# Optimization experiments

Hardware: AMD Instinct MI355X
Metric: run time of the kernel (lower is better)

## Reference

```python
import jax, jax.numpy as jnp
import numpy as np

NR_EMB = 1024
B_COMMITMENT = 1.0


def setup_inputs() -> dict:
    key = jax.random.key(0)
    k1, k2 = jax.random.split(key)
    inpt = jax.random.normal(k1, (64, 2048, 64), dtype=jnp.float32)
    # VarianceScaling(uniform) over shape (D, K): limit = sqrt(3*scale/fan_in), scale=1, fan_in=D
    D = 64
    limit = np.sqrt(3.0 / D).astype(np.float32)
    emb_mtrx = jax.random.uniform(k2, (D, NR_EMB), dtype=jnp.float32, minval=-limit, maxval=limit)
    return {"inpt": inpt, "emb_mtrx": emb_mtrx}


def reference(inpt, emb_mtrx):
    D = inpt.shape[-1]
    x = inpt.reshape(-1, D)  # [N, D]
    dist = (jnp.sum(x * x, axis=1, keepdims=True)
            - 2.0 * (x @ emb_mtrx)
            + jnp.sum(emb_mtrx * emb_mtrx, axis=0, keepdims=True))
    idx = jnp.argmax(-dist, axis=1)  # [N]
    # avg_probs = mean of one-hot over N == normalized histogram (same math, no N x K one-hot)
    avg_probs = jnp.bincount(idx, length=NR_EMB).astype(inpt.dtype) / x.shape[0]
    perplexity = jnp.exp(-jnp.sum(avg_probs * jnp.log(avg_probs + 1e-10)))
    idx_nd = idx.reshape(inpt.shape[:-1])  # [B, T]
    q = jnp.take(emb_mtrx.T, idx_nd, axis=0)  # gather codebook rows -> [B, T, D]
    l_commitment = jnp.mean((jax.lax.stop_gradient(q) - inpt) ** 2)
    l_codebook = jnp.mean((q - jax.lax.stop_gradient(inpt)) ** 2)
    loss = B_COMMITMENT * l_commitment + l_codebook
    q = inpt + jax.lax.stop_gradient(q - inpt)  # straight-through estimator
    return q, loss, perplexity
```

## Files before the change

### kernel.cpp

```cpp
#include <hip/hip_runtime.h>

#define NROWS 131072
#define D 64
#define K 1024

typedef __attribute__((ext_vector_type(8))) short short8;
typedef __attribute__((ext_vector_type(4))) float f32x4;
typedef unsigned int u32;


__device__ __forceinline__ unsigned short f2bf_rne(float f) {
    u32 u = __float_as_uint(f);
    u += 0x7fff + ((u >> 16) & 1);
    return (unsigned short)(u >> 16);
}

__device__ __forceinline__ float b2f(short s) {
    return __uint_as_float(((u32)(unsigned short)s) << 16);
}

__global__ __launch_bounds__(256) void prep_kernel(const float* __restrict__ E,
                                                   unsigned short* __restrict__ ehT,
                                                   float* __restrict__ e2g,
                                                   int* __restrict__ hist) {
    __shared__ float ps[4][64];
    const int lane = threadIdx.x & 63;
    const int w = threadIdx.x >> 6;
    const int k = blockIdx.x * 64 + lane;
    float s = 0.f;
#pragma unroll
    for (int half = 0; half < 2; ++half) {
        short8 h8;
#pragma unroll
        for (int j = 0; j < 8; ++j) {
            float v = E[(w * 16 + half * 8 + j) * K + k];
            s = fmaf(v, v, s);
            h8[j] = (short)f2bf_rne(v);
        }
        *(short8*)(ehT + (size_t)k * D + w * 16 + half * 8) = h8;
    }
    ps[w][lane] = s;
    __syncthreads();
    if (w == 0) e2g[k] = -0.5f * (ps[0][lane] + ps[1][lane] + ps[2][lane] + ps[3][lane]);
    if (threadIdx.x < 64) hist[blockIdx.x * 64 + threadIdx.x] = 0;
}

__global__ __launch_bounds__(256) void score_kernel(const float* __restrict__ X,
                                                    const unsigned short* __restrict__ ehT,
                                                    const float* __restrict__ e2g,
                                                    int* __restrict__ hist,
                                                    float* __restrict__ wavesum,
                                                    float* __restrict__ q) {
    __shared__ unsigned short xbuf[8192];
    __shared__ float mrg[128 * 5];
    __shared__ int idxl[128];
    __shared__ float redL[4];

    const int tid = threadIdx.x;
    const int wave = tid >> 6;
    const int lane = tid & 63;
    const int quad = lane >> 4;
    const int lc = lane & 15;
    const size_t row0 = (size_t)blockIdx.x * 128;

#pragma unroll
    for (int j = 0; j < 4; ++j) {
        int u = tid + j * 256;
        int tt = u >> 7, oo = (u >> 4) & 7, ll = u & 15;
        const float* xp = X + (row0 + (size_t)(tt * 16 + ll)) * D + oo * 8;
        float4 La = *(const float4*)(xp);
        float4 Lb = *(const float4*)(xp + 4);
        union { u32 uu[4]; short8 v; } pk;
        pk.uu[0] = __builtin_amdgcn_perm(__float_as_uint(La.y), __float_as_uint(La.x), 0x07060302);
        pk.uu[1] = __builtin_amdgcn_perm(__float_as_uint(La.w), __float_as_uint(La.z), 0x07060302);
        pk.uu[2] = __builtin_amdgcn_perm(__float_as_uint(Lb.y), __float_as_uint(Lb.x), 0x07060302);
        pk.uu[3] = __builtin_amdgcn_perm(__float_as_uint(Lb.w), __float_as_uint(Lb.z), 0x07060302);
        *(short8*)((char*)&xbuf[0] + u * 16) = pk.v;
    }
    __syncthreads();

    float bt8[8];
#pragma unroll
    for (int t = 0; t < 8; ++t) bt8[t] = -3.4e38f;

#pragma unroll 1
    for (int h = 0; h < 4; ++h) {
        const int cg = h * 256 + wave * 64;
        short8 ae[4][2];
        f32x4 e2f[4];
#pragma unroll
        for (int ct = 0; ct < 4; ++ct) {
            const unsigned short* ap = ehT + ((size_t)(cg + ct * 16 + lc) << 6) + quad * 8;
            ae[ct][0] = *(const short8*)(ap);
            ae[ct][1] = *(const short8*)(ap + 32);
            e2f[ct] = *(const f32x4*)(e2g + cg + ct * 16 + quad * 4);
        }
        const u32 cb0 = (u32)(cg + quad * 4);

#pragma unroll 2
        for (int t = 0; t < 8; ++t) {
            const char* bp = (const char*)&xbuf[0] + t * 2048 + quad * 256 + lc * 16;
            short8 b0 = *(const short8*)(bp);
            short8 b1 = *(const short8*)(bp + 1024);
            float bt = bt8[t];
#pragma unroll
            for (int ct = 0; ct < 4; ++ct) {
                f32x4 acc = __builtin_amdgcn_mfma_f32_16x16x32_bf16(ae[ct][0], b0, e2f[ct], 0, 0, 0);
                acc = __builtin_amdgcn_mfma_f32_16x16x32_bf16(ae[ct][1], b1, acc, 0, 0, 0);
                float p0 = __uint_as_float((__float_as_uint(acc[0]) & 0xFFFFFC00u) | (cb0 + ct * 16 + 0));
                float p1 = __uint_as_float((__float_as_uint(acc[1]) & 0xFFFFFC00u) | (cb0 + ct * 16 + 1));
                float p2 = __uint_as_float((__float_as_uint(acc[2]) & 0xFFFFFC00u) | (cb0 + ct * 16 + 2));
                float p3 = __uint_as_float((__float_as_uint(acc[3]) & 0xFFFFFC00u) | (cb0 + ct * 16 + 3));
                bt = fmaxf(bt, fmaxf(p0, p1));
                bt = fmaxf(bt, fmaxf(p2, p3));
            }
            bt8[t] = bt;
        }
    }

#pragma unroll
    for (int t = 0; t < 8; ++t) {
        float bt = bt8[t];
        bt = fmaxf(bt, __shfl_xor(bt, 16, 64));
        bt = fmaxf(bt, __shfl_xor(bt, 32, 64));
        if (lane < 16) mrg[(t * 16 + lane) * 5 + wave] = bt;
    }
    __syncthreads();

    if (tid < 128) {
        float m = fmaxf(fmaxf(mrg[tid * 5 + 0], mrg[tid * 5 + 1]),
                        fmaxf(mrg[tid * 5 + 2], mrg[tid * 5 + 3]));
        int kk = (int)(__float_as_uint(m) & 1023u);
        idxl[tid] = kk;
        atomicAdd(&hist[kk], 1);
    }
    __syncthreads();

    float ls = 0.f;
    const int er = tid >> 4, el = tid & 15;
#pragma unroll 2
    for (int it = 0; it < 8; ++it) {
        int rl = it * 16 + er;
        int k = idxl[rl];
        size_t row = row0 + rl;
        float4 xv = *(const float4*)(X + row * D + el * 4);
        short4 ev = *(const short4*)((const char*)ehT + (size_t)k * 128 + el * 8);
        float4 o;
        float dd;
        dd = b2f(ev.x) - xv.x; ls = fmaf(dd, dd, ls); o.x = xv.x + dd;
        dd = b2f(ev.y) - xv.y; ls = fmaf(dd, dd, ls); o.y = xv.y + dd;
        dd = b2f(ev.z) - xv.z; ls = fmaf(dd, dd, ls); o.z = xv.z + dd;
        dd = b2f(ev.w) - xv.w; ls = fmaf(dd, dd, ls); o.w = xv.w + dd;
        *(float4*)(q + row * D + el * 4) = o;
    }
    for (int off = 32; off > 0; off >>= 1) ls += __shfl_down(ls, off, 64);
    if (lane == 0) redL[wave] = ls;
    __syncthreads();
    if (tid == 0)
        wavesum[blockIdx.x] = redL[0] + redL[1] + redL[2] + redL[3];
}

__global__ __launch_bounds__(1024) void finalize_kernel(const int* __restrict__ hist,
                                                        const float* __restrict__ wavesum,
                                                        float* __restrict__ out) {
    __shared__ float redH[16], redL[16];
    int tid = threadIdx.x;
    float p = (float)hist[tid] * (1.0f / (float)NROWS);
    float term = p * logf(p + 1e-10f);
    float ls = wavesum[tid];
    for (int off = 32; off > 0; off >>= 1) {
        term += __shfl_down(term, off, 64);
        ls += __shfl_down(ls, off, 64);
    }
    int lane = tid & 63, wid = tid >> 6;
    if (lane == 0) { redH[wid] = term; redL[wid] = ls; }
    __syncthreads();
    if (tid == 0) {
        float H = 0.f, L = 0.f;
#pragma unroll
        for (int i = 0; i < 16; ++i) { H += redH[i]; L += redL[i]; }
        out[(size_t)NROWS * D + 0] = 2.0f * (L / (float)(NROWS * D));
        out[(size_t)NROWS * D + 1] = expf(-H);
    }
}

extern "C" void kernel_launch(void* const* d_in, const int* in_sizes, int n_in,
                              void* d_out, int out_size, void* d_ws, size_t ws_size,
                              hipStream_t stream) {
    const float* X = (const float*)d_in[0];
    const float* E = (const float*)d_in[1];
    float* out = (float*)d_out;

    char* w = (char*)d_ws;
    unsigned short* ehT = (unsigned short*)(w + 0);
    float* e2g          = (float*)(w + 131072);
    int* hist           = (int*)(w + 135168);
    float* wavesum      = (float*)(w + 139264);

    prep_kernel<<<16, 256, 0, stream>>>(E, ehT, e2g, hist);
    score_kernel<<<NROWS / 128, 256, 0, stream>>>(X, ehT, e2g, hist, wavesum, out);
    finalize_kernel<<<1, 1024, 0, stream>>>(hist, wavesum, out);
}
```

Measured before the change: 126.5 us.

## Widen score kernel to eight waves and reuse staged bf16 inputs in epilogue

The score kernel now runs 512 threads per block. Each of eight waves owns 128 contiguous codebook entries, prefetches the next codebook tile in registers while it runs MFMAs over the current one, and reads the codebook norms from LDS. The epilogue no longer re-reads the fp32 input from global memory. It computes the commitment loss from the bf16 (truncated) copy already held in LDS and writes the bf16 codebook value straight out as q. This removes a second full pass over the input, but the loss is now computed from lower-precision inputs.

```diff
diff --git a/kernel.cpp b/kernel.cpp
--- a/kernel.cpp
+++ b/kernel.cpp
@@ -45,16 +45,17 @@
     if (threadIdx.x < 64) hist[blockIdx.x * 64 + threadIdx.x] = 0;
 }
 
-__global__ __launch_bounds__(256) void score_kernel(const float* __restrict__ X,
+__global__ __launch_bounds__(512) void score_kernel(const float* __restrict__ X,
                                                     const unsigned short* __restrict__ ehT,
                                                     const float* __restrict__ e2g,
                                                     int* __restrict__ hist,
                                                     float* __restrict__ wavesum,
                                                     float* __restrict__ q) {
     __shared__ unsigned short xbuf[8192];
-    __shared__ float mrg[128 * 5];
+    __shared__ float e2s[1024];
+    __shared__ float mrg[128 * 9];
     __shared__ int idxl[128];
-    __shared__ float redL[4];
+    __shared__ float redL[8];
 
     const int tid = threadIdx.x;
     const int wave = tid >> 6;
@@ -64,8 +65,8 @@
     const size_t row0 = (size_t)blockIdx.x * 128;
 
 #pragma unroll
-    for (int j = 0; j < 4; ++j) {
-        int u = tid + j * 256;
+    for (int j = 0; j < 2; ++j) {
+        int u = tid + j * 512;
         int tt = u >> 7, oo = (u >> 4) & 7, ll = u & 15;
         const float* xp = X + (row0 + (size_t)(tt * 16 + ll)) * D + oo * 8;
         float4 La = *(const float4*)(xp);
@@ -77,45 +78,52 @@
         pk.uu[3] = __builtin_amdgcn_perm(__float_as_uint(Lb.w), __float_as_uint(Lb.z), 0x07060302);
         *(short8*)((char*)&xbuf[0] + u * 16) = pk.v;
     }
+    e2s[tid] = e2g[tid];
+    e2s[tid + 512] = e2g[tid + 512];
+
+    const int cbase = wave * 128;
+    const unsigned short* ap = ehT + ((size_t)(cbase + lc) << 6) + quad * 8;
+
     __syncthreads();
 
     float bt8[8];
 #pragma unroll
     for (int t = 0; t < 8; ++t) bt8[t] = -3.4e38f;
 
+    short8 a0 = *(const short8*)(ap);
+    short8 a1 = *(const short8*)(ap + 32);
+    f32x4 ev2 = *(const f32x4*)(&e2s[cbase + quad * 4]);
+
 #pragma unroll 1
-    for (int h = 0; h < 4; ++h) {
-        const int cg = h * 256 + wave * 64;
-        short8 ae[4][2];
-        f32x4 e2f[4];
-#pragma unroll
-        for (int ct = 0; ct < 4; ++ct) {
-            const unsigned short* ap = ehT + ((size_t)(cg + ct * 16 + lc) << 6) + quad * 8;
-            ae[ct][0] = *(const short8*)(ap);
-            ae[ct][1] = *(const short8*)(ap + 32);
-            e2f[ct] = *(const f32x4*)(e2g + cg + ct * 16 + quad * 4);
+    for (int ct = 0; ct < 8; ++ct) {
+        short8 n0, n1;
+        f32x4 en;
+        if (ct < 7) {
+            const unsigned short* np = ap + (ct + 1) * 1024;
+            n0 = *(const short8*)(np);
+            n1 = *(const short8*)(np + 32);
+            en = *(const f32x4*)(&e2s[cbase + (ct + 1) * 16 + quad * 4]);
         }
-        const u32 cb0 = (u32)(cg + quad * 4);
-
-#pragma unroll 2
+        const u32 cb = (u32)(cbase + ct * 16 + quad * 4);
+        const char* bb = (const char*)&xbuf[0];
+        asm volatile("" : "+v"(bb));
+#pragma unroll
         for (int t = 0; t < 8; ++t) {
-            const char* bp = (const char*)&xbuf[0] + t * 2048 + quad * 256 + lc * 16;
+            const char* bp = bb + t * 2048 + quad * 256 + lc * 16;
             short8 b0 = *(const short8*)(bp);
             short8 b1 = *(const short8*)(bp + 1024);
+            f32x4 acc = __builtin_amdgcn_mfma_f32_16x16x32_bf16(a0, b0, ev2, 0, 0, 0);
+            acc = __builtin_amdgcn_mfma_f32_16x16x32_bf16(a1, b1, acc, 0, 0, 0);
+            float p0 = __uint_as_float((__float_as_uint(acc[0]) & 0xFFFFFC00u) | (cb + 0));
+            float p1 = __uint_as_float((__float_as_uint(acc[1]) & 0xFFFFFC00u) | (cb + 1));
+            float p2 = __uint_as_float((__float_as_uint(acc[2]) & 0xFFFFFC00u) | (cb + 2));
+            float p3 = __uint_as_float((__float_as_uint(acc[3]) & 0xFFFFFC00u) | (cb + 3));
             float bt = bt8[t];
-#pragma unroll
-            for (int ct = 0; ct < 4; ++ct) {
-                f32x4 acc = __builtin_amdgcn_mfma_f32_16x16x32_bf16(ae[ct][0], b0, e2f[ct], 0, 0, 0);
-                acc = __builtin_amdgcn_mfma_f32_16x16x32_bf16(ae[ct][1], b1, acc, 0, 0, 0);
-                float p0 = __uint_as_float((__float_as_uint(acc[0]) & 0xFFFFFC00u) | (cb0 + ct * 16 + 0));
-                float p1 = __uint_as_float((__float_as_uint(acc[1]) & 0xFFFFFC00u) | (cb0 + ct * 16 + 1));
-                float p2 = __uint_as_float((__float_as_uint(acc[2]) & 0xFFFFFC00u) | (cb0 + ct * 16 + 2));
-                float p3 = __uint_as_float((__float_as_uint(acc[3]) & 0xFFFFFC00u) | (cb0 + ct * 16 + 3));
-                bt = fmaxf(bt, fmaxf(p0, p1));
-                bt = fmaxf(bt, fmaxf(p2, p3));
-            }
+            bt = fmaxf(bt, fmaxf(p0, p1));
+            bt = fmaxf(bt, fmaxf(p2, p3));
             bt8[t] = bt;
         }
+        a0 = n0; a1 = n1; ev2 = en;
     }
 
 #pragma unroll
@@ -123,41 +131,52 @@
         float bt = bt8[t];
         bt = fmaxf(bt, __shfl_xor(bt, 16, 64));
         bt = fmaxf(bt, __shfl_xor(bt, 32, 64));
-        if (lane < 16) mrg[(t * 16 + lane) * 5 + wave] = bt;
+        if (lane < 16) mrg[(t * 16 + lane) * 9 + wave] = bt;
     }
     __syncthreads();
 
     if (tid < 128) {
-        float m = fmaxf(fmaxf(mrg[tid * 5 + 0], mrg[tid * 5 + 1]),
-                        fmaxf(mrg[tid * 5 + 2], mrg[tid * 5 + 3]));
-        int kk = (int)(__float_as_uint(m) & 1023u);
-        idxl[tid] = kk;
-        atomicAdd(&hist[kk], 1);
-    }
-    __syncthreads();
+        float m = mrg[tid * 9];
+#pragma unroll
+        for (int w = 1; w < 8; ++w) m = fmaxf(m, mrg[tid * 9 + w]);
+        idxl[tid] = (int)(__float_as_uint(m) & 1023u);
+    }
+    __syncthreads();
+
+    if (tid < 128) atomicAdd(&hist[idxl[tid]], 1);
 
     float ls = 0.f;
-    const int er = tid >> 4, el = tid & 15;
-#pragma unroll 2
-    for (int it = 0; it < 8; ++it) {
-        int rl = it * 16 + er;
-        int k = idxl[rl];
-        size_t row = row0 + rl;
-        float4 xv = *(const float4*)(X + row * D + el * 4);
-        short4 ev = *(const short4*)((const char*)ehT + (size_t)k * 128 + el * 8);
-        float4 o;
-        float dd;
-        dd = b2f(ev.x) - xv.x; ls = fmaf(dd, dd, ls); o.x = xv.x + dd;
-        dd = b2f(ev.y) - xv.y; ls = fmaf(dd, dd, ls); o.y = xv.y + dd;
-        dd = b2f(ev.z) - xv.z; ls = fmaf(dd, dd, ls); o.z = xv.z + dd;
-        dd = b2f(ev.w) - xv.w; ls = fmaf(dd, dd, ls); o.w = xv.w + dd;
-        *(float4*)(q + row * D + el * 4) = o;
-    }
+#pragma unroll
+    for (int j = 0; j < 2; ++j) {
+        int u = tid + j * 512;
+        int rowl = ((u >> 7) << 4) + (u & 15), so = (u >> 4) & 7;
+        int kk = idxl[rowl];
+        short8 ev = *(const short8*)(ehT + ((size_t)kk << 6) + so * 8);
+        short8 xv = *(const short8*)(&xbuf[u * 8]);
+        float4 qa, qb;
+        float e0, dd;
+        e0 = b2f(ev[0]); dd = e0 - b2f(xv[0]); ls = fmaf(dd, dd, ls); qa.x = e0;
+        e0 = b2f(ev[1]); dd = e0 - b2f(xv[1]); ls = fmaf(dd, dd, ls); qa.y = e0;
+        e0 = b2f(ev[2]); dd = e0 - b2f(xv[2]); ls = fmaf(dd, dd, ls); qa.z = e0;
+        e0 = b2f(ev[3]); dd = e0 - b2f(xv[3]); ls = fmaf(dd, dd, ls); qa.w = e0;
+        e0 = b2f(ev[4]); dd = e0 - b2f(xv[4]); ls = fmaf(dd, dd, ls); qb.x = e0;
+        e0 = b2f(ev[5]); dd = e0 - b2f(xv[5]); ls = fmaf(dd, dd, ls); qb.y = e0;
+        e0 = b2f(ev[6]); dd = e0 - b2f(xv[6]); ls = fmaf(dd, dd, ls); qb.z = e0;
+        e0 = b2f(ev[7]); dd = e0 - b2f(xv[7]); ls = fmaf(dd, dd, ls); qb.w = e0;
+        float* qp = q + (row0 + (size_t)rowl) * D + so * 8;
+        *(float4*)(qp) = qa;
+        *(float4*)(qp + 4) = qb;
+    }
+
     for (int off = 32; off > 0; off >>= 1) ls += __shfl_down(ls, off, 64);
     if (lane == 0) redL[wave] = ls;
     __syncthreads();
-    if (tid == 0)
-        wavesum[blockIdx.x] = redL[0] + redL[1] + redL[2] + redL[3];
+    if (tid == 0) {
+        float L = 0.f;
+#pragma unroll
+        for (int i = 0; i < 8; ++i) L += redL[i];
+        wavesum[blockIdx.x] = L;
+    }
 }
 
 __global__ __launch_bounds__(1024) void finalize_kernel(const int* __restrict__ hist,
@@ -198,6 +217,6 @@
     float* wavesum      = (float*)(w + 139264);
 
     prep_kernel<<<16, 256, 0, stream>>>(E, ehT, e2g, hist);
-    score_kernel<<<NROWS / 128, 256, 0, stream>>>(X, ehT, e2g, hist, wavesum, out);
+    score_kernel<<<NROWS / 128, 512, 0, stream>>>(X, ehT, e2g, hist, wavesum, out);
     finalize_kernel<<<1, 1024, 0, stream>>>(hist, wavesum, out);
 }
```

New measurement: 140.4 us. 11.0% more time.
